# Performance work log

Measured on AMD Instinct MI355X. Metric: run time of the kernel, lower is better.

## Reference

```python
import jax, jax.numpy as jnp
import numpy as np

B, L, D = 8, 4096, 256
G, K = 64, 8          # n_groups, group_size
N = G * K             # 512 slots
H = 8                 # attention heads
EPS = 1e-5

def _ln(x, g, b):
    m = jnp.mean(x, axis=-1, keepdims=True)
    v = jnp.var(x, axis=-1, keepdims=True)
    return (x - m) * jax.lax.rsqrt(v + EPS) * g + b

def _gelu(x):
    return jax.nn.gelu(x, approximate=False)  # torch nn.GELU default = exact erf

def setup_inputs() -> dict:
    key = jax.random.key(0)
    ks = jax.random.split(key, 24)
    s = 0.02
    d = {
        'X': jax.random.normal(ks[0], (B, L, D), jnp.float32),
        'S': jax.random.normal(ks[1], (B, N, D), jnp.float32),
        'Wg':  jax.random.normal(ks[2], (D, G)) * s,
        'Wk':  jax.random.normal(ks[3], (D, K)) * s,
        'Wm1': jax.random.normal(ks[4], (D, 2*D)) * s, 'bm1': jnp.zeros((2*D,)),
        'Wm2': jax.random.normal(ks[5], (2*D, D)) * s, 'bm2': jnp.zeros((D,)),
        'Wgt1': jax.random.normal(ks[6], (D, D)) * s, 'bgt1': jnp.zeros((D,)),
        'Wgt2': jax.random.normal(ks[7], (D, 1)) * s, 'bgt2': jnp.zeros((1,)),
        'Wqkv': jax.random.normal(ks[8], (D, 3*D)) * s, 'bqkv': jnp.zeros((3*D,)),
        'Wo':  jax.random.normal(ks[9], (D, D)) * s, 'bo': jnp.zeros((D,)),
        'aln_g': jnp.ones((D,)), 'aln_b': jnp.zeros((D,)),
        'Wu1': jax.random.normal(ks[10], (2*D, 2*D)) * s, 'bu1': jnp.zeros((2*D,)),
        'Wu2': jax.random.normal(ks[11], (2*D, D)) * s, 'bu2': jnp.zeros((D,)),
        'ln_g': jnp.ones((D,)), 'ln_b': jnp.zeros((D,)),
    }
    return d

def reference(X, S, Wg, Wk, Wm1, bm1, Wm2, bm2, Wgt1, bgt1, Wgt2, bgt2,
              Wqkv, bqkv, Wo, bo, aln_g, aln_b, Wu1, bu1, Wu2, bu2, ln_g, ln_b):
    # --- hierarchical routing (eval path: argmax one-hot) ---
    msg = _gelu(X @ Wm1 + bm1) @ Wm2 + bm2                 # (B,L,D)
    gate = jax.nn.sigmoid(_gelu(X @ Wgt1 + bgt1) @ Wgt2 + bgt2)  # (B,L,1)
    gm = msg * gate
    gidx = jnp.argmax(X @ Wg, axis=-1)                     # (B,L)
    kidx = jnp.argmax(X @ Wk, axis=-1)                     # (B,L)
    idx = gidx * K + kidx                                  # flat slot id in [0,N)
    full = jax.nn.one_hot(idx, N, dtype=X.dtype)           # (B,L,N)
    incoming = jnp.einsum('bln,bld->bnd', full, gm)        # (B,N,D)
    # --- slot self-attention ---
    qkv = S @ Wqkv + bqkv
    q, k, v = jnp.split(qkv, 3, axis=-1)
    dh = D // H
    q = q.reshape(B, N, H, dh); k = k.reshape(B, N, H, dh); v = v.reshape(B, N, H, dh)
    scores = jnp.einsum('bqhd,bkhd->bhqk', q, k) / jnp.sqrt(jnp.asarray(dh, X.dtype))
    attn = jax.nn.softmax(scores, axis=-1)
    o = jnp.einsum('bhqk,bkhd->bqhd', attn, v).reshape(B, N, D) @ Wo + bo
    S1 = _ln(S + o, aln_g, aln_b)
    # --- update ---
    cat = jnp.concatenate([S1, incoming], axis=-1)         # (B,N,2D)
    S2 = S1 + _gelu(cat @ Wu1 + bu1) @ Wu2 + bu2
    return _ln(S2, ln_g, ln_b)
```

## Files before the change

kernel.cpp:

```cpp
#include <hip/hip_runtime.h>

typedef __bf16 bf16_t;
typedef __bf16 bf16x8 __attribute__((ext_vector_type(8)));
typedef __bf16 bf16x4v __attribute__((ext_vector_type(4)));
typedef __bf16 bf16x2v __attribute__((ext_vector_type(2)));
typedef float f32x4 __attribute__((ext_vector_type(4)));
typedef unsigned long long u64;

#define LN_EPS 1e-5f

__device__ __forceinline__ float erf_fast(float a) {
  const float t = fabsf(a);
  const float s = a * a;
  float r;
  if (t > 0.921875f) {
    float u;
    r = fmaf(-1.72853470e-5f, t, 3.83197126e-4f);
    u = fmaf(-3.88396438e-3f, t, 2.42546219e-2f);
    r = fmaf(r, s, u);
    r = fmaf(r, t, 1.06777877e-1f);
    r = fmaf(r, t, -6.37245935e-1f);
    r = fmaf(r, t, -1.28717512e-1f);
    r = fmaf(r, t, t);
    r = 1.0f - __expf(-r);
    r = copysignf(r, a);
  } else {
    r = -5.96761703e-4f;
    r = fmaf(r, s, 4.99119423e-3f);
    r = fmaf(r, s, -2.67681349e-2f);
    r = fmaf(r, s, 1.12819925e-1f);
    r = fmaf(r, s, -3.76125336e-1f);
    r = fmaf(r, s, 1.28379166e-1f);
    r = fmaf(r, a, a);
  }
  return r;
}

__device__ __forceinline__ float gelu_f(float x) {
  const float h = 0.5f * x;
  return fmaf(h, erf_fast(x * 0.70710678118654752f), h);
}

__device__ __forceinline__ void async16(const bf16_t* g, bf16_t* l) {
  __builtin_amdgcn_global_load_lds(
      (const __attribute__((address_space(1))) void*)g,
      (__attribute__((address_space(3))) void*)l, 16, 0, 0);
}

__global__ __launch_bounds__(256)
void prep_kernel(const float* __restrict__ X, const float* __restrict__ S,
                 const float* __restrict__ Wg, const float* __restrict__ Wk,
                 const float* __restrict__ Wm1, const float* __restrict__ Wgt1,
                 const float* __restrict__ Wm2, const float* __restrict__ Wqkv,
                 const float* __restrict__ Wo, const float* __restrict__ Wu1,
                 const float* __restrict__ Wu2,
                 bf16_t* __restrict__ Xb, bf16_t* __restrict__ Sb,
                 bf16_t* __restrict__ W1t, bf16_t* __restrict__ W2t,
                 bf16_t* __restrict__ Wqkvt, bf16_t* __restrict__ Wot,
                 bf16_t* __restrict__ Wu1t, bf16_t* __restrict__ Wu2t,
                 float4* __restrict__ zbase)
{
  const int bid = blockIdx.x;
  const int t = threadIdx.x;
  if (bid < 8192) {
    const int i = bid * 256 + t;
    const float4 v = ((const float4*)X)[i];
    bf16x4v o; o[0]=(bf16_t)v.x; o[1]=(bf16_t)v.y; o[2]=(bf16_t)v.z; o[3]=(bf16_t)v.w;
    ((bf16x4v*)Xb)[i] = o;
  } else if (bid < 9216) {
    const int i = (bid - 8192) * 256 + t;
    const float4 v = ((const float4*)S)[i];
    bf16x4v o; o[0]=(bf16_t)v.x; o[1]=(bf16_t)v.y; o[2]=(bf16_t)v.z; o[3]=(bf16_t)v.w;
    ((bf16x4v*)Sb)[i] = o;
  } else if (bid < 10112) {
    const int n = bid - 9216;
    const int k = t;
    float v;
    if (n < 512)      v = Wm1[k * 512 + n];
    else if (n < 768) v = Wgt1[k * 256 + (n - 512)];
    else if (n < 832) v = Wg[k * 64 + (n - 768)];
    else if (n < 840) v = Wk[k * 8 + (n - 832)];
    else              v = 0.f;
    W1t[n * 256 + k] = (bf16_t)v;
  } else if (bid < 10368) {
    const int n = bid - 10112;
    for (int k = t; k < 512; k += 256) W2t[n * 512 + k] = (bf16_t)Wm2[k * 256 + n];
  } else if (bid < 11136) {
    const int n = bid - 10368;
    Wqkvt[n * 256 + t] = (bf16_t)Wqkv[t * 768 + n];
  } else if (bid < 11392) {
    const int n = bid - 11136;
    Wot[n * 256 + t] = (bf16_t)Wo[t * 256 + n];
  } else if (bid < 11904) {
    const int n = bid - 11392;
    for (int k = t; k < 512; k += 256) Wu1t[n * 512 + k] = (bf16_t)Wu1[k * 512 + n];
  } else if (bid < 12160) {
    const int n = bid - 11904;
    for (int k = t; k < 512; k += 256) Wu2t[n * 512 + k] = (bf16_t)Wu2[k * 256 + n];
  } else {
    zbase[(bid - 12160) * 256 + t] = make_float4(0.f, 0.f, 0.f, 0.f);
  }
}

template<int MT, int EPI>
__global__ __launch_bounds__(256)
void gemm_kernel(const bf16_t* __restrict__ A, int lda,
                 const bf16_t* __restrict__ Bt, int K,
                 const float* __restrict__ bias, const float* __restrict__ bias2,
                 void* __restrict__ outp, int ldc,
                 const float* __restrict__ resid, const float* __restrict__ wgt2,
                 float* __restrict__ gatelin, int* __restrict__ idxb,
                 u64* __restrict__ bitmap)
{
  constexpr int BM = MT * 32;
  constexpr int CA = BM * 4;
  const int m0 = blockIdx.x * BM;
  const int by = blockIdx.y;
  const int n0 = by * 128;
  const int t = threadIdx.x;
  const int w = t >> 6;
  const int lane = t & 63;
  const int wr = w >> 1, wc = w & 1;
  const int quad = lane >> 4, l15 = lane & 15;

  __shared__ bf16_t lA[BM * 32];
  __shared__ bf16_t lB[128 * 32];
  __shared__ float sWg[256];
  __shared__ int sKi[128];

  if constexpr (EPI == 1) {
    if (by >= 4 && by < 6) sWg[t] = wgt2[t];
  }

  f32x4 acc[MT][4];
#pragma unroll
  for (int mt = 0; mt < MT; ++mt)
#pragma unroll
    for (int nt = 0; nt < 4; ++nt)
      acc[mt][nt] = (f32x4){0.f, 0.f, 0.f, 0.f};

  for (int k0 = 0; k0 < K; k0 += 32) {
    if constexpr (CA >= 256) {
#pragma unroll
      for (int i = 0; i < CA / 256; ++i) {
        const int c = i * 256 + t;
        async16(A + (size_t)(m0 + (c >> 2)) * lda + k0 + (c & 3) * 8,
                lA + (size_t)(i * 256 + (t & 192)) * 8);
      }
    } else {
      if (t < CA)
        async16(A + (size_t)(m0 + (t >> 2)) * lda + k0 + (t & 3) * 8,
                lA + (size_t)(t & 192) * 8);
    }
#pragma unroll
    for (int i = 0; i < 2; ++i) {
      const int c = i * 256 + t;
      async16(Bt + (size_t)(n0 + (c >> 2)) * K + k0 + (c & 3) * 8,
              lB + (size_t)(i * 256 + (t & 192)) * 8);
    }
    __syncthreads();
    bf16x8 af[MT], bfr[4];
    const int ko = quad * 8;
#pragma unroll
    for (int mt = 0; mt < MT; ++mt)
      af[mt] = *(const bf16x8*)&lA[(wr * MT * 16 + mt * 16 + l15) * 32 + ko];
#pragma unroll
    for (int nt = 0; nt < 4; ++nt)
      bfr[nt] = *(const bf16x8*)&lB[(wc * 64 + nt * 16 + l15) * 32 + ko];
#pragma unroll
    for (int mt = 0; mt < MT; ++mt)
#pragma unroll
      for (int nt = 0; nt < 4; ++nt)
        acc[mt][nt] = __builtin_amdgcn_mfma_f32_16x16x32_bf16(bfr[nt], af[mt], acc[mt][nt], 0, 0, 0);
    __syncthreads();
  }

  if constexpr (EPI == 1) {
    if (by < 4) {
#pragma unroll
      for (int mt = 0; mt < MT; ++mt) {
        const int row = m0 + wr * MT * 16 + mt * 16 + l15;
#pragma unroll
        for (int nt = 0; nt < 4; ++nt) {
          const int colb = n0 + wc * 64 + nt * 16 + quad * 4;
          const float4 bb = *(const float4*)&bias[colb];
          bf16x4v o;
          o[0] = (bf16_t)gelu_f(acc[mt][nt][0] + bb.x);
          o[1] = (bf16_t)gelu_f(acc[mt][nt][1] + bb.y);
          o[2] = (bf16_t)gelu_f(acc[mt][nt][2] + bb.z);
          o[3] = (bf16_t)gelu_f(acc[mt][nt][3] + bb.w);
          *(bf16x4v*)&((bf16_t*)outp)[(size_t)row * 512 + colb] = o;
        }
      }
    } else if (by < 6) {
#pragma unroll
      for (int mt = 0; mt < MT; ++mt) {
        const int row = m0 + wr * MT * 16 + mt * 16 + l15;
        float part = 0.f;
#pragma unroll
        for (int nt = 0; nt < 4; ++nt) {
          const int colb = n0 + wc * 64 + nt * 16 + quad * 4;
          const int c = colb - 512;
          const float4 bb = *(const float4*)&bias2[c];
          part = fmaf(gelu_f(acc[mt][nt][0] + bb.x), sWg[c + 0], part);
          part = fmaf(gelu_f(acc[mt][nt][1] + bb.y), sWg[c + 1], part);
          part = fmaf(gelu_f(acc[mt][nt][2] + bb.z), sWg[c + 2], part);
          part = fmaf(gelu_f(acc[mt][nt][3] + bb.w), sWg[c + 3], part);
        }
        part += __shfl_xor(part, 16, 64);
        part += __shfl_xor(part, 32, 64);
        if (lane < 16) atomicAdd(&gatelin[row], part);
      }
    } else {
      float bv[MT]; int bi[MT];
#pragma unroll
      for (int mt = 0; mt < MT; ++mt) {
        if (wc == 0) {
          float mv = -1e30f; int mi = 0;
#pragma unroll
          for (int nt = 0; nt < 4; ++nt)
#pragma unroll
            for (int j = 0; j < 4; ++j) {
              const int gc = nt * 16 + quad * 4 + j;
              const float v = acc[mt][nt][j];
              if (v > mv || (v == mv && gc < mi)) { mv = v; mi = gc; }
            }
#pragma unroll
          for (int off = 16; off <= 32; off <<= 1) {
            const float ov = __shfl_xor(mv, off, 64);
            const int oi = __shfl_xor(mi, off, 64);
            if (ov > mv || (ov == mv && oi < mi)) { mv = ov; mi = oi; }
          }
          bv[mt] = mv; bi[mt] = mi;
        } else {
          float mv = -1e30f; int mi = 0;
          if (quad < 2) {
#pragma unroll
            for (int j = 0; j < 4; ++j) {
              const int kc = quad * 4 + j;
              const float v = acc[mt][0][j];
              if (v > mv || (v == mv && kc < mi)) { mv = v; mi = kc; }
            }
          }
#pragma unroll
          for (int off = 16; off <= 32; off <<= 1) {
            const float ov = __shfl_xor(mv, off, 64);
            const int oi = __shfl_xor(mi, off, 64);
            if (ov > mv || (ov == mv && oi < mi)) { mv = ov; mi = oi; }
          }
          if (lane < 16) sKi[wr * MT * 16 + mt * 16 + l15] = mi;
        }
      }
      __syncthreads();
      if (wc == 0 && lane < 16) {
#pragma unroll
        for (int mt = 0; mt < MT; ++mt) {
          const int rl = wr * MT * 16 + mt * 16 + l15;
          const int row = m0 + rl;
          const int idx = bi[mt] * 8 + sKi[rl];
          idxb[row] = idx;
          const int b = row >> 12, tok = row & 4095;
          atomicOr(&bitmap[(size_t)(b * 512 + idx) * 64 + (tok >> 6)],
                   1ull << (tok & 63));
        }
      }
    }
  } else {
#pragma unroll
    for (int mt = 0; mt < MT; ++mt) {
      const int row = m0 + wr * MT * 16 + mt * 16 + l15;
#pragma unroll
      for (int nt = 0; nt < 4; ++nt) {
        const int colb = n0 + wc * 64 + nt * 16 + quad * 4;
        const float4 bb = *(const float4*)&bias[colb];
        float v0 = acc[mt][nt][0] + bb.x, v1 = acc[mt][nt][1] + bb.y;
        float v2 = acc[mt][nt][2] + bb.z, v3 = acc[mt][nt][3] + bb.w;
        if constexpr (EPI == 4) {
          *(float4*)&((float*)outp)[(size_t)row * ldc + colb] = make_float4(v0, v1, v2, v3);
        } else if constexpr (EPI == 5) {
          bf16x4v o; o[0]=(bf16_t)gelu_f(v0); o[1]=(bf16_t)gelu_f(v1);
          o[2]=(bf16_t)gelu_f(v2); o[3]=(bf16_t)gelu_f(v3);
          *(bf16x4v*)&((bf16_t*)outp)[(size_t)row * ldc + colb] = o;
        } else {
          const float4 rr = *(const float4*)&resid[(size_t)row * ldc + colb];
          *(float4*)&((float*)outp)[(size_t)row * ldc + colb] =
              make_float4(v0 + rr.x, v1 + rr.y, v2 + rr.z, v3 + rr.w);
        }
      }
    }
  }
}

__global__ __launch_bounds__(256)
void gemm_pair_kernel(const bf16_t* __restrict__ H, const bf16_t* __restrict__ W2t,
                      const float* __restrict__ bm2, const float* __restrict__ sumg,
                      float* __restrict__ incom,
                      const bf16_t* __restrict__ Sb, const bf16_t* __restrict__ Wqkvt,
                      const float* __restrict__ bqkv, bf16_t* __restrict__ qkvb)
{
  int id = blockIdx.x;
  const bool first = id < 256;
  if (!first) id -= 256;
  const bf16_t* A  = first ? H : Sb;
  const bf16_t* Bt = first ? W2t : Wqkvt;
  const float* bias = first ? bm2 : bqkv;
  const int lda = first ? 512 : 256;
  const int K   = first ? 512 : 256;
  const int ldc = first ? 256 : 768;
  const int m0 = (id & 127) * 32;
  const int n0 = (id >> 7) * 128;
  const int t = threadIdx.x;
  const int w = t >> 6;
  const int lane = t & 63;
  const int wr = w >> 1, wc = w & 1;
  const int quad = lane >> 4, l15 = lane & 15;

  __shared__ bf16_t lA[32 * 32];
  __shared__ bf16_t lB[128 * 32];

  f32x4 acc[4];
#pragma unroll
  for (int nt = 0; nt < 4; ++nt) acc[nt] = (f32x4){0.f, 0.f, 0.f, 0.f};

  for (int k0 = 0; k0 < K; k0 += 32) {
    if (t < 128)
      async16(A + (size_t)(m0 + (t >> 2)) * lda + k0 + (t & 3) * 8,
              lA + (size_t)(t & 192) * 8);
#pragma unroll
    for (int i = 0; i < 2; ++i) {
      const int c = i * 256 + t;
      async16(Bt + (size_t)(n0 + (c >> 2)) * K + k0 + (c & 3) * 8,
              lB + (size_t)(i * 256 + (t & 192)) * 8);
    }
    __syncthreads();
    bf16x8 af, bfr[4];
    const int ko = quad * 8;
    af = *(const bf16x8*)&lA[(wr * 16 + l15) * 32 + ko];
#pragma unroll
    for (int nt = 0; nt < 4; ++nt)
      bfr[nt] = *(const bf16x8*)&lB[(wc * 64 + nt * 16 + l15) * 32 + ko];
#pragma unroll
    for (int nt = 0; nt < 4; ++nt)
      acc[nt] = __builtin_amdgcn_mfma_f32_16x16x32_bf16(bfr[nt], af, acc[nt], 0, 0, 0);
    __syncthreads();
  }

  const int row = m0 + wr * 16 + l15;
  if (first) {
    const float gt = sumg[row];
#pragma unroll
    for (int nt = 0; nt < 4; ++nt) {
      const int colb = n0 + wc * 64 + nt * 16 + quad * 4;
      const float4 bb = *(const float4*)&bias[colb];
      *(float4*)&incom[(size_t)row * ldc + colb] =
          make_float4(fmaf(gt, bb.x, acc[nt][0]), fmaf(gt, bb.y, acc[nt][1]),
                      fmaf(gt, bb.z, acc[nt][2]), fmaf(gt, bb.w, acc[nt][3]));
    }
  } else {
#pragma unroll
    for (int nt = 0; nt < 4; ++nt) {
      const int colb = n0 + wc * 64 + nt * 16 + quad * 4;
      const float4 bb = *(const float4*)&bias[colb];
      bf16x4v o; o[0]=(bf16_t)(acc[nt][0]+bb.x); o[1]=(bf16_t)(acc[nt][1]+bb.y);
      o[2]=(bf16_t)(acc[nt][2]+bb.z); o[3]=(bf16_t)(acc[nt][3]+bb.w);
      *(bf16x4v*)&qkvb[(size_t)row * ldc + colb] = o;
    }
  }
}

__global__ __launch_bounds__(256)
void gather_kernel(const bf16_t* __restrict__ h1, const float* __restrict__ gatelin,
                   const float* __restrict__ bgt2, const u64* __restrict__ bitmap,
                   bf16_t* __restrict__ H, float* __restrict__ sumg)
{
  const int bs = blockIdx.x;
  const int b = bs >> 9;
  const int t = threadIdx.x;
  __shared__ u64 sw[64];
  if (t < 64) sw[t] = bitmap[(size_t)bs * 64 + t];
  __syncthreads();
  const float bg = bgt2[0];
  float a0 = 0.f, a1 = 0.f, sg = 0.f;
  for (int wd = 0; wd < 64; ++wd) {
    u64 word = sw[wd];
    while (word) {
      const int bit = __builtin_ctzll(word);
      word &= word - 1;
      const int l = (b << 12) + (wd << 6) + bit;
      const float g = 1.0f / (1.0f + __expf(-(gatelin[l] + bg)));
      const bf16x2v hv = *(const bf16x2v*)&h1[(size_t)l * 512 + t * 2];
      a0 = fmaf(g, (float)hv[0], a0);
      a1 = fmaf(g, (float)hv[1], a1);
      sg += g;
    }
  }
  bf16x2v o; o[0] = (bf16_t)a0; o[1] = (bf16_t)a1;
  *(bf16x2v*)&H[(size_t)bs * 512 + t * 2] = o;
  if (t == 0) sumg[bs] = sg;
}

__global__ __launch_bounds__(256)
void attn_kernel(const bf16_t* __restrict__ qkv, bf16_t* __restrict__ obuf)
{
  const int bid = blockIdx.x;
  const int qc = bid & 15;
  const int h = (bid >> 4) & 7;
  const int b = bid >> 7;
  const int t = threadIdx.x;
  const int w = t >> 6, lane = t & 63;
  const int quad = lane >> 4, l15 = lane & 15;

  __shared__ bf16_t sP[32 * 520];
  __shared__ bf16_t sVt[32 * 264];
  __shared__ float sL[32];

  bf16x8 qf[2];
#pragma unroll
  for (int mt = 0; mt < 2; ++mt) {
    const int row = b * 512 + qc * 32 + mt * 16 + l15;
    qf[mt] = *(const bf16x8*)&qkv[(size_t)row * 768 + h * 32 + quad * 8];
  }
  const float scale = 0.17677669529663687f;
  for (int kt = w; kt < 32; kt += 4) {
    const int key = b * 512 + kt * 16 + l15;
    const bf16x8 kf = *(const bf16x8*)&qkv[(size_t)key * 768 + 256 + h * 32 + quad * 8];
#pragma unroll
    for (int mt = 0; mt < 2; ++mt) {
      f32x4 c = (f32x4){0.f, 0.f, 0.f, 0.f};
      c = __builtin_amdgcn_mfma_f32_16x16x32_bf16(qf[mt], kf, c, 0, 0, 0);
#pragma unroll
      for (int r = 0; r < 4; ++r)
        sP[(mt * 16 + quad * 4 + r) * 520 + kt * 16 + l15] = (bf16_t)(c[r] * scale);
    }
  }
  __syncthreads();

#pragma unroll
  for (int ri = 0; ri < 8; ++ri) {
    const int row = w * 8 + ri;
    const bf16x8 sv = *(const bf16x8*)&sP[row * 520 + lane * 8];
    float sval[8];
    float mx = -1e30f;
#pragma unroll
    for (int j = 0; j < 8; ++j) { sval[j] = (float)sv[j]; mx = fmaxf(mx, sval[j]); }
#pragma unroll
    for (int off = 32; off; off >>= 1) mx = fmaxf(mx, __shfl_xor(mx, off, 64));
    float sum = 0.f;
    bf16x8 pv;
#pragma unroll
    for (int j = 0; j < 8; ++j) { const float e = __expf(sval[j] - mx); sum += e; pv[j] = (bf16_t)e; }
#pragma unroll
    for (int off = 32; off; off >>= 1) sum += __shfl_xor(sum, off, 64);
    *(bf16x8*)&sP[row * 520 + lane * 8] = pv;
    if (lane == 0) sL[row] = sum;
  }
  __syncthreads();

  const int omt = w >> 1, ont = w & 1;
  f32x4 oacc = (f32x4){0.f, 0.f, 0.f, 0.f};
  for (int half = 0; half < 2; ++half) {
    if (half) __syncthreads();
#pragma unroll
    for (int i = 0; i < 32; ++i) {
      const int el = i * 256 + t;
      const int dh = el & 31, key = el >> 5;
      sVt[dh * 264 + key] = qkv[(size_t)(b * 512 + half * 256 + key) * 768 + 512 + h * 32 + dh];
    }
    __syncthreads();
#pragma unroll
    for (int kt = 0; kt < 8; ++kt) {
      const bf16x8 af = *(const bf16x8*)&sP[(omt * 16 + l15) * 520 + half * 256 + kt * 32 + quad * 8];
      const bf16x8 vf = *(const bf16x8*)&sVt[(ont * 16 + l15) * 264 + kt * 32 + quad * 8];
      oacc = __builtin_amdgcn_mfma_f32_16x16x32_bf16(af, vf, oacc, 0, 0, 0);
    }
  }
#pragma unroll
  for (int r = 0; r < 4; ++r) {
    const int row = omt * 16 + quad * 4 + r;
    const float val = oacc[r] / sL[row];
    obuf[(size_t)(b * 512 + qc * 32 + row) * 256 + h * 32 + ont * 16 + l15] = (bf16_t)val;
  }
}

__global__ __launch_bounds__(256)
void ln1_kernel(const float* __restrict__ S, const float* __restrict__ o2,
                const float* __restrict__ incom, const float* __restrict__ g,
                const float* __restrict__ bb, float* __restrict__ S1f,
                bf16_t* __restrict__ A4)
{
  const int w = threadIdx.x >> 6, lane = threadIdx.x & 63;
  const int row = blockIdx.x * 4 + w;
  const size_t base = (size_t)row * 256 + lane * 4;
  const float4 xs = *(const float4*)&S[base];
  const float4 xo = *(const float4*)&o2[base];
  float x[4] = {xs.x + xo.x, xs.y + xo.y, xs.z + xo.z, xs.w + xo.w};
  float sum = x[0] + x[1] + x[2] + x[3];
  float sq = x[0]*x[0] + x[1]*x[1] + x[2]*x[2] + x[3]*x[3];
#pragma unroll
  for (int off = 32; off; off >>= 1) { sum += __shfl_xor(sum, off, 64); sq += __shfl_xor(sq, off, 64); }
  const float mean = sum * 0.00390625f;
  const float var = sq * 0.00390625f - mean * mean;
  const float rstd = rsqrtf(var + LN_EPS);
  const float4 gg = *(const float4*)&g[lane * 4];
  const float4 bv = *(const float4*)&bb[lane * 4];
  float y[4];
  y[0] = (x[0]-mean)*rstd*gg.x + bv.x;
  y[1] = (x[1]-mean)*rstd*gg.y + bv.y;
  y[2] = (x[2]-mean)*rstd*gg.z + bv.z;
  y[3] = (x[3]-mean)*rstd*gg.w + bv.w;
  *(float4*)&S1f[base] = make_float4(y[0], y[1], y[2], y[3]);
  bf16x4v yb; yb[0]=(bf16_t)y[0]; yb[1]=(bf16_t)y[1]; yb[2]=(bf16_t)y[2]; yb[3]=(bf16_t)y[3];
  *(bf16x4v*)&A4[(size_t)row * 512 + lane * 4] = yb;
  const float4 ic = *(const float4*)&incom[base];
  bf16x4v ib; ib[0]=(bf16_t)ic.x; ib[1]=(bf16_t)ic.y; ib[2]=(bf16_t)ic.z; ib[3]=(bf16_t)ic.w;
  *(bf16x4v*)&A4[(size_t)row * 512 + 256 + lane * 4] = ib;
}

__global__ __launch_bounds__(256)
void ln2_kernel(const float* __restrict__ S2, const float* __restrict__ g,
                const float* __restrict__ bb, float* __restrict__ out)
{
  const int w = threadIdx.x >> 6, lane = threadIdx.x & 63;
  const int row = blockIdx.x * 4 + w;
  const size_t base = (size_t)row * 256 + lane * 4;
  const float4 xv = *(const float4*)&S2[base];
  float x[4] = {xv.x, xv.y, xv.z, xv.w};
  float sum = x[0] + x[1] + x[2] + x[3];
  float sq = x[0]*x[0] + x[1]*x[1] + x[2]*x[2] + x[3]*x[3];
#pragma unroll
  for (int off = 32; off; off >>= 1) { sum += __shfl_xor(sum, off, 64); sq += __shfl_xor(sq, off, 64); }
  const float mean = sum * 0.00390625f;
  const float var = sq * 0.00390625f - mean * mean;
  const float rstd = rsqrtf(var + LN_EPS);
  const float4 gg = *(const float4*)&g[lane * 4];
  const float4 bv = *(const float4*)&bb[lane * 4];
  float4 o;
  o.x = (x[0]-mean)*rstd*gg.x + bv.x;
  o.y = (x[1]-mean)*rstd*gg.y + bv.y;
  o.z = (x[2]-mean)*rstd*gg.z + bv.z;
  o.w = (x[3]-mean)*rstd*gg.w + bv.w;
  *(float4*)&out[base] = o;
}

extern "C" void kernel_launch(void* const* d_in, const int* in_sizes, int n_in,
                              void* d_out, int out_size, void* d_ws, size_t ws_size,
                              hipStream_t stream)
{
  (void)in_sizes; (void)n_in; (void)out_size; (void)ws_size;
  const float* X    = (const float*)d_in[0];
  const float* S    = (const float*)d_in[1];
  const float* Wg   = (const float*)d_in[2];
  const float* Wk   = (const float*)d_in[3];
  const float* Wm1  = (const float*)d_in[4];
  const float* bm1  = (const float*)d_in[5];
  const float* Wm2  = (const float*)d_in[6];
  const float* bm2  = (const float*)d_in[7];
  const float* Wgt1 = (const float*)d_in[8];
  const float* bgt1 = (const float*)d_in[9];
  const float* Wgt2 = (const float*)d_in[10];
  const float* bgt2 = (const float*)d_in[11];
  const float* Wqkv = (const float*)d_in[12];
  const float* bqkv = (const float*)d_in[13];
  const float* Wo   = (const float*)d_in[14];
  const float* bo   = (const float*)d_in[15];
  const float* alng = (const float*)d_in[16];
  const float* alnb = (const float*)d_in[17];
  const float* Wu1  = (const float*)d_in[18];
  const float* bu1  = (const float*)d_in[19];
  const float* Wu2  = (const float*)d_in[20];
  const float* bu2  = (const float*)d_in[21];
  const float* lng  = (const float*)d_in[22];
  const float* lnb  = (const float*)d_in[23];

  char* p = (char*)d_ws;
  auto carve = [&](size_t bytes) { char* r = p; p += bytes; return r; };
  bf16_t* Xb    = (bf16_t*)carve(16777216);
  bf16_t* Sb    = (bf16_t*)carve(2097152);
  bf16_t* W1t   = (bf16_t*)carve(458752);
  bf16_t* W2t   = (bf16_t*)carve(262144);
  bf16_t* Wqkvt = (bf16_t*)carve(393216);
  bf16_t* Wot   = (bf16_t*)carve(131072);
  bf16_t* Wu1t  = (bf16_t*)carve(524288);
  bf16_t* Wu2t  = (bf16_t*)carve(262144);
  bf16_t* h1    = (bf16_t*)carve(33554432);
  u64*    bitmap  = (u64*)carve(2097152);
  float*  gatelin = (float*)carve(131072);
  int*    idxb  = (int*)carve(131072);
  float*  incom = (float*)carve(4194304);
  bf16_t* qkvb  = (bf16_t*)carve(6291456);
  bf16_t* obuf  = (bf16_t*)carve(2097152);
  float*  o2    = (float*)carve(4194304);
  float*  S1f   = (float*)carve(4194304);
  bf16_t* A4    = (bf16_t*)carve(4194304);
  bf16_t* U     = (bf16_t*)carve(4194304);
  float*  S2    = (float*)carve(4194304);
  float*  sumg  = (float*)carve(16384);
  bf16_t* H = U;

  prep_kernel<<<12704, 256, 0, stream>>>(X, S, Wg, Wk, Wm1, Wgt1, Wm2, Wqkv, Wo, Wu1, Wu2,
                                         Xb, Sb, W1t, W2t, Wqkvt, Wot, Wu1t, Wu2t,
                                         (float4*)bitmap);
  gemm_kernel<4,1><<<dim3(256,7), 256, 0, stream>>>(Xb, 256, W1t, 256, bm1, bgt1, h1, 512,
                                                    nullptr, Wgt2, gatelin, idxb, bitmap);
  gather_kernel<<<4096, 256, 0, stream>>>(h1, gatelin, bgt2, bitmap, H, sumg);
  gemm_pair_kernel<<<1024, 256, 0, stream>>>(H, W2t, bm2, sumg, incom,
                                             Sb, Wqkvt, bqkv, qkvb);
  attn_kernel<<<1024, 256, 0, stream>>>(qkvb, obuf);
  gemm_kernel<1,4><<<dim3(128,2), 256, 0, stream>>>(obuf, 256, Wot, 256, bo, nullptr, o2, 256,
                                                    nullptr, nullptr, nullptr, nullptr, nullptr);
  ln1_kernel<<<1024, 256, 0, stream>>>(S, o2, incom, alng, alnb, S1f, A4);
  gemm_kernel<1,5><<<dim3(128,4), 256, 0, stream>>>(A4, 512, Wu1t, 512, bu1, nullptr, U, 512,
                                                    nullptr, nullptr, nullptr, nullptr, nullptr);
  gemm_kernel<1,6><<<dim3(128,2), 256, 0, stream>>>(U, 512, Wu2t, 512, bu2, nullptr, S2, 256,
                                                    S1f, nullptr, nullptr, nullptr, nullptr);
  ln2_kernel<<<1024, 256, 0, stream>>>(S2, lng, lnb, (float*)d_out);
}
```

Before: 271.8 us.

## Fuse Wo and Wu2 GEMMs with their LayerNorms and shrink routing GEMM tile

Replaces the Wo GEMM plus ln1 kernel, and the Wu2 GEMM plus ln2 kernel, with two fused kernels. Each fused kernel computes a 16-row by full-256-column tile so the LayerNorm row reduction runs in the GEMM epilogue, which removes the o2 and S2 intermediate round trips and two launches. The first routing GEMM moves from MT=4 to MT=2 tiles, doubling its grid. The unused idxb output is dropped. The fused kernels launch only 256 blocks with single-buffered loads, which may underuse the GPU.

```diff
diff --git a/kernel.cpp b/kernel.cpp
--- a/kernel.cpp
+++ b/kernel.cpp
@@ -108,8 +108,7 @@
                  const bf16_t* __restrict__ Bt, int K,
                  const float* __restrict__ bias, const float* __restrict__ bias2,
                  void* __restrict__ outp, int ldc,
-                 const float* __restrict__ resid, const float* __restrict__ wgt2,
-                 float* __restrict__ gatelin, int* __restrict__ idxb,
+                 const float* __restrict__ wgt2, float* __restrict__ gatelin,
                  u64* __restrict__ bitmap)
 {
   constexpr int BM = MT * 32;
@@ -126,7 +125,7 @@
   __shared__ bf16_t lA[BM * 32];
   __shared__ bf16_t lB[128 * 32];
   __shared__ float sWg[256];
-  __shared__ int sKi[128];
+  __shared__ int sKi[BM];
 
   if constexpr (EPI == 1) {
     if (by >= 4 && by < 6) sWg[t] = wgt2[t];
@@ -212,7 +211,7 @@
         if (lane < 16) atomicAdd(&gatelin[row], part);
       }
     } else {
-      float bv[MT]; int bi[MT];
+      int bi[MT];
 #pragma unroll
       for (int mt = 0; mt < MT; ++mt) {
         if (wc == 0) {
@@ -231,7 +230,7 @@
             const int oi = __shfl_xor(mi, off, 64);
             if (ov > mv || (ov == mv && oi < mi)) { mv = ov; mi = oi; }
           }
-          bv[mt] = mv; bi[mt] = mi;
+          bi[mt] = mi;
         } else {
           float mv = -1e30f; int mi = 0;
           if (quad < 2) {
@@ -258,7 +257,6 @@
           const int rl = wr * MT * 16 + mt * 16 + l15;
           const int row = m0 + rl;
           const int idx = bi[mt] * 8 + sKi[rl];
-          idxb[row] = idx;
           const int b = row >> 12, tok = row & 4095;
           atomicOr(&bitmap[(size_t)(b * 512 + idx) * 64 + (tok >> 6)],
                    1ull << (tok & 63));
@@ -273,19 +271,10 @@
       for (int nt = 0; nt < 4; ++nt) {
         const int colb = n0 + wc * 64 + nt * 16 + quad * 4;
         const float4 bb = *(const float4*)&bias[colb];
-        float v0 = acc[mt][nt][0] + bb.x, v1 = acc[mt][nt][1] + bb.y;
-        float v2 = acc[mt][nt][2] + bb.z, v3 = acc[mt][nt][3] + bb.w;
-        if constexpr (EPI == 4) {
-          *(float4*)&((float*)outp)[(size_t)row * ldc + colb] = make_float4(v0, v1, v2, v3);
-        } else if constexpr (EPI == 5) {
-          bf16x4v o; o[0]=(bf16_t)gelu_f(v0); o[1]=(bf16_t)gelu_f(v1);
-          o[2]=(bf16_t)gelu_f(v2); o[3]=(bf16_t)gelu_f(v3);
-          *(bf16x4v*)&((bf16_t*)outp)[(size_t)row * ldc + colb] = o;
-        } else {
-          const float4 rr = *(const float4*)&resid[(size_t)row * ldc + colb];
-          *(float4*)&((float*)outp)[(size_t)row * ldc + colb] =
-              make_float4(v0 + rr.x, v1 + rr.y, v2 + rr.z, v3 + rr.w);
-        }
+        bf16x4v o;
+        o[0]=(bf16_t)gelu_f(acc[mt][nt][0]+bb.x); o[1]=(bf16_t)gelu_f(acc[mt][nt][1]+bb.y);
+        o[2]=(bf16_t)gelu_f(acc[mt][nt][2]+bb.z); o[3]=(bf16_t)gelu_f(acc[mt][nt][3]+bb.w);
+        *(bf16x4v*)&((bf16_t*)outp)[(size_t)row * ldc + colb] = o;
       }
     }
   }
@@ -483,63 +472,157 @@
 }
 
 __global__ __launch_bounds__(256)
-void ln1_kernel(const float* __restrict__ S, const float* __restrict__ o2,
-                const float* __restrict__ incom, const float* __restrict__ g,
-                const float* __restrict__ bb, float* __restrict__ S1f,
-                bf16_t* __restrict__ A4)
-{
-  const int w = threadIdx.x >> 6, lane = threadIdx.x & 63;
-  const int row = blockIdx.x * 4 + w;
-  const size_t base = (size_t)row * 256 + lane * 4;
-  const float4 xs = *(const float4*)&S[base];
-  const float4 xo = *(const float4*)&o2[base];
-  float x[4] = {xs.x + xo.x, xs.y + xo.y, xs.z + xo.z, xs.w + xo.w};
-  float sum = x[0] + x[1] + x[2] + x[3];
-  float sq = x[0]*x[0] + x[1]*x[1] + x[2]*x[2] + x[3]*x[3];
-#pragma unroll
-  for (int off = 32; off; off >>= 1) { sum += __shfl_xor(sum, off, 64); sq += __shfl_xor(sq, off, 64); }
-  const float mean = sum * 0.00390625f;
-  const float var = sq * 0.00390625f - mean * mean;
+void wo_ln1_kernel(const bf16_t* __restrict__ obuf, const bf16_t* __restrict__ Wot,
+                   const float* __restrict__ bo, const float* __restrict__ S,
+                   const float* __restrict__ incom, const float* __restrict__ g,
+                   const float* __restrict__ bb, float* __restrict__ S1f,
+                   bf16_t* __restrict__ A4)
+{
+  const int m0 = blockIdx.x * 16;
+  const int t = threadIdx.x;
+  const int w = t >> 6, lane = t & 63;
+  const int quad = lane >> 4, l15 = lane & 15;
+
+  __shared__ bf16_t lA[16 * 32];
+  __shared__ bf16_t lB[256 * 32];
+  __shared__ float sSum[4][16];
+  __shared__ float sSq[4][16];
+
+  f32x4 acc[4];
+#pragma unroll
+  for (int nt = 0; nt < 4; ++nt) acc[nt] = (f32x4){0.f, 0.f, 0.f, 0.f};
+
+  for (int k0 = 0; k0 < 256; k0 += 32) {
+    if (t < 64)
+      async16(obuf + (size_t)(m0 + (t >> 2)) * 256 + k0 + (t & 3) * 8, lA);
+#pragma unroll
+    for (int i = 0; i < 4; ++i) {
+      const int c = i * 256 + t;
+      async16(Wot + (size_t)(c >> 2) * 256 + k0 + (c & 3) * 8,
+              lB + (size_t)(i * 256 + (t & 192)) * 8);
+    }
+    __syncthreads();
+    const int ko = quad * 8;
+    const bf16x8 af = *(const bf16x8*)&lA[l15 * 32 + ko];
+#pragma unroll
+    for (int nt = 0; nt < 4; ++nt) {
+      const bf16x8 bfr = *(const bf16x8*)&lB[(w * 64 + nt * 16 + l15) * 32 + ko];
+      acc[nt] = __builtin_amdgcn_mfma_f32_16x16x32_bf16(bfr, af, acc[nt], 0, 0, 0);
+    }
+    __syncthreads();
+  }
+
+  const int row = m0 + l15;
+  float sum = 0.f, sq = 0.f;
+#pragma unroll
+  for (int nt = 0; nt < 4; ++nt) {
+    const int colb = w * 64 + nt * 16 + quad * 4;
+    const float4 bv = *(const float4*)&bo[colb];
+    const float4 sv = *(const float4*)&S[(size_t)row * 256 + colb];
+    float x0 = acc[nt][0] + bv.x + sv.x, x1 = acc[nt][1] + bv.y + sv.y;
+    float x2 = acc[nt][2] + bv.z + sv.z, x3 = acc[nt][3] + bv.w + sv.w;
+    acc[nt][0] = x0; acc[nt][1] = x1; acc[nt][2] = x2; acc[nt][3] = x3;
+    sum += x0 + x1 + x2 + x3;
+    sq += x0*x0 + x1*x1 + x2*x2 + x3*x3;
+  }
+  sum += __shfl_xor(sum, 16, 64); sum += __shfl_xor(sum, 32, 64);
+  sq  += __shfl_xor(sq, 16, 64);  sq  += __shfl_xor(sq, 32, 64);
+  if (lane < 16) { sSum[w][l15] = sum; sSq[w][l15] = sq; }
+  __syncthreads();
+  const float tot = sSum[0][l15] + sSum[1][l15] + sSum[2][l15] + sSum[3][l15];
+  const float tq  = sSq[0][l15] + sSq[1][l15] + sSq[2][l15] + sSq[3][l15];
+  const float mean = tot * 0.00390625f;
+  const float var = tq * 0.00390625f - mean * mean;
   const float rstd = rsqrtf(var + LN_EPS);
-  const float4 gg = *(const float4*)&g[lane * 4];
-  const float4 bv = *(const float4*)&bb[lane * 4];
-  float y[4];
-  y[0] = (x[0]-mean)*rstd*gg.x + bv.x;
-  y[1] = (x[1]-mean)*rstd*gg.y + bv.y;
-  y[2] = (x[2]-mean)*rstd*gg.z + bv.z;
-  y[3] = (x[3]-mean)*rstd*gg.w + bv.w;
-  *(float4*)&S1f[base] = make_float4(y[0], y[1], y[2], y[3]);
-  bf16x4v yb; yb[0]=(bf16_t)y[0]; yb[1]=(bf16_t)y[1]; yb[2]=(bf16_t)y[2]; yb[3]=(bf16_t)y[3];
-  *(bf16x4v*)&A4[(size_t)row * 512 + lane * 4] = yb;
-  const float4 ic = *(const float4*)&incom[base];
-  bf16x4v ib; ib[0]=(bf16_t)ic.x; ib[1]=(bf16_t)ic.y; ib[2]=(bf16_t)ic.z; ib[3]=(bf16_t)ic.w;
-  *(bf16x4v*)&A4[(size_t)row * 512 + 256 + lane * 4] = ib;
+#pragma unroll
+  for (int nt = 0; nt < 4; ++nt) {
+    const int colb = w * 64 + nt * 16 + quad * 4;
+    const float4 gg = *(const float4*)&g[colb];
+    const float4 bv = *(const float4*)&bb[colb];
+    const float y0 = (acc[nt][0]-mean)*rstd*gg.x + bv.x;
+    const float y1 = (acc[nt][1]-mean)*rstd*gg.y + bv.y;
+    const float y2 = (acc[nt][2]-mean)*rstd*gg.z + bv.z;
+    const float y3 = (acc[nt][3]-mean)*rstd*gg.w + bv.w;
+    *(float4*)&S1f[(size_t)row * 256 + colb] = make_float4(y0, y1, y2, y3);
+    bf16x4v yb; yb[0]=(bf16_t)y0; yb[1]=(bf16_t)y1; yb[2]=(bf16_t)y2; yb[3]=(bf16_t)y3;
+    *(bf16x4v*)&A4[(size_t)row * 512 + colb] = yb;
+    const float4 ic = *(const float4*)&incom[(size_t)row * 256 + colb];
+    bf16x4v ib; ib[0]=(bf16_t)ic.x; ib[1]=(bf16_t)ic.y; ib[2]=(bf16_t)ic.z; ib[3]=(bf16_t)ic.w;
+    *(bf16x4v*)&A4[(size_t)row * 512 + 256 + colb] = ib;
+  }
 }
 
 __global__ __launch_bounds__(256)
-void ln2_kernel(const float* __restrict__ S2, const float* __restrict__ g,
-                const float* __restrict__ bb, float* __restrict__ out)
-{
-  const int w = threadIdx.x >> 6, lane = threadIdx.x & 63;
-  const int row = blockIdx.x * 4 + w;
-  const size_t base = (size_t)row * 256 + lane * 4;
-  const float4 xv = *(const float4*)&S2[base];
-  float x[4] = {xv.x, xv.y, xv.z, xv.w};
-  float sum = x[0] + x[1] + x[2] + x[3];
-  float sq = x[0]*x[0] + x[1]*x[1] + x[2]*x[2] + x[3]*x[3];
-#pragma unroll
-  for (int off = 32; off; off >>= 1) { sum += __shfl_xor(sum, off, 64); sq += __shfl_xor(sq, off, 64); }
-  const float mean = sum * 0.00390625f;
-  const float var = sq * 0.00390625f - mean * mean;
+void wu2_ln2_kernel(const bf16_t* __restrict__ U, const bf16_t* __restrict__ Wu2t,
+                    const float* __restrict__ bu2, const float* __restrict__ S1f,
+                    const float* __restrict__ g, const float* __restrict__ bb,
+                    float* __restrict__ out)
+{
+  const int m0 = blockIdx.x * 16;
+  const int t = threadIdx.x;
+  const int w = t >> 6, lane = t & 63;
+  const int quad = lane >> 4, l15 = lane & 15;
+
+  __shared__ bf16_t lA[16 * 32];
+  __shared__ bf16_t lB[256 * 32];
+  __shared__ float sSum[4][16];
+  __shared__ float sSq[4][16];
+
+  f32x4 acc[4];
+#pragma unroll
+  for (int nt = 0; nt < 4; ++nt) acc[nt] = (f32x4){0.f, 0.f, 0.f, 0.f};
+
+  for (int k0 = 0; k0 < 512; k0 += 32) {
+    if (t < 64)
+      async16(U + (size_t)(m0 + (t >> 2)) * 512 + k0 + (t & 3) * 8, lA);
+#pragma unroll
+    for (int i = 0; i < 4; ++i) {
+      const int c = i * 256 + t;
+      async16(Wu2t + (size_t)(c >> 2) * 512 + k0 + (c & 3) * 8,
+              lB + (size_t)(i * 256 + (t & 192)) * 8);
+    }
+    __syncthreads();
+    const int ko = quad * 8;
+    const bf16x8 af = *(const bf16x8*)&lA[l15 * 32 + ko];
+#pragma unroll
+    for (int nt = 0; nt < 4; ++nt) {
+      const bf16x8 bfr = *(const bf16x8*)&lB[(w * 64 + nt * 16 + l15) * 32 + ko];
+      acc[nt] = __builtin_amdgcn_mfma_f32_16x16x32_bf16(bfr, af, acc[nt], 0, 0, 0);
+    }
+    __syncthreads();
+  }
+
+  const int row = m0 + l15;
+  float sum = 0.f, sq = 0.f;
+#pragma unroll
+  for (int nt = 0; nt < 4; ++nt) {
+    const int colb = w * 64 + nt * 16 + quad * 4;
+    const float4 bv = *(const float4*)&bu2[colb];
+    const float4 sv = *(const float4*)&S1f[(size_t)row * 256 + colb];
+    float x0 = acc[nt][0] + bv.x + sv.x, x1 = acc[nt][1] + bv.y + sv.y;
+    float x2 = acc[nt][2] + bv.z + sv.z, x3 = acc[nt][3] + bv.w + sv.w;
+    acc[nt][0] = x0; acc[nt][1] = x1; acc[nt][2] = x2; acc[nt][3] = x3;
+    sum += x0 + x1 + x2 + x3;
+    sq += x0*x0 + x1*x1 + x2*x2 + x3*x3;
+  }
+  sum += __shfl_xor(sum, 16, 64); sum += __shfl_xor(sum, 32, 64);
+  sq  += __shfl_xor(sq, 16, 64);  sq  += __shfl_xor(sq, 32, 64);
+  if (lane < 16) { sSum[w][l15] = sum; sSq[w][l15] = sq; }
+  __syncthreads();
+  const float tot = sSum[0][l15] + sSum[1][l15] + sSum[2][l15] + sSum[3][l15];
+  const float tq  = sSq[0][l15] + sSq[1][l15] + sSq[2][l15] + sSq[3][l15];
+  const float mean = tot * 0.00390625f;
+  const float var = tq * 0.00390625f - mean * mean;
   const float rstd = rsqrtf(var + LN_EPS);
-  const float4 gg = *(const float4*)&g[lane * 4];
-  const float4 bv = *(const float4*)&bb[lane * 4];
-  float4 o;
-  o.x = (x[0]-mean)*rstd*gg.x + bv.x;
-  o.y = (x[1]-mean)*rstd*gg.y + bv.y;
-  o.z = (x[2]-mean)*rstd*gg.z + bv.z;
-  o.w = (x[3]-mean)*rstd*gg.w + bv.w;
-  *(float4*)&out[base] = o;
+#pragma unroll
+  for (int nt = 0; nt < 4; ++nt) {
+    const int colb = w * 64 + nt * 16 + quad * 4;
+    const float4 gg = *(const float4*)&g[colb];
+    const float4 bv = *(const float4*)&bb[colb];
+    *(float4*)&out[(size_t)row * 256 + colb] = make_float4(
+        (acc[nt][0]-mean)*rstd*gg.x + bv.x, (acc[nt][1]-mean)*rstd*gg.y + bv.y,
+        (acc[nt][2]-mean)*rstd*gg.z + bv.z, (acc[nt][3]-mean)*rstd*gg.w + bv.w);
+  }
 }
 
 extern "C" void kernel_launch(void* const* d_in, const int* in_sizes, int n_in,
@@ -585,33 +668,26 @@
   bf16_t* h1    = (bf16_t*)carve(33554432);
   u64*    bitmap  = (u64*)carve(2097152);
   float*  gatelin = (float*)carve(131072);
-  int*    idxb  = (int*)carve(131072);
   float*  incom = (float*)carve(4194304);
   bf16_t* qkvb  = (bf16_t*)carve(6291456);
   bf16_t* obuf  = (bf16_t*)carve(2097152);
-  float*  o2    = (float*)carve(4194304);
   float*  S1f   = (float*)carve(4194304);
   bf16_t* A4    = (bf16_t*)carve(4194304);
   bf16_t* U     = (bf16_t*)carve(4194304);
-  float*  S2    = (float*)carve(4194304);
   float*  sumg  = (float*)carve(16384);
   bf16_t* H = U;
 
   prep_kernel<<<12704, 256, 0, stream>>>(X, S, Wg, Wk, Wm1, Wgt1, Wm2, Wqkv, Wo, Wu1, Wu2,
                                          Xb, Sb, W1t, W2t, Wqkvt, Wot, Wu1t, Wu2t,
                                          (float4*)bitmap);
-  gemm_kernel<4,1><<<dim3(256,7), 256, 0, stream>>>(Xb, 256, W1t, 256, bm1, bgt1, h1, 512,
-                                                    nullptr, Wgt2, gatelin, idxb, bitmap);
+  gemm_kernel<2,1><<<dim3(512,7), 256, 0, stream>>>(Xb, 256, W1t, 256, bm1, bgt1, h1, 512,
+                                                    Wgt2, gatelin, bitmap);
   gather_kernel<<<4096, 256, 0, stream>>>(h1, gatelin, bgt2, bitmap, H, sumg);
   gemm_pair_kernel<<<1024, 256, 0, stream>>>(H, W2t, bm2, sumg, incom,
                                              Sb, Wqkvt, bqkv, qkvb);
   attn_kernel<<<1024, 256, 0, stream>>>(qkvb, obuf);
-  gemm_kernel<1,4><<<dim3(128,2), 256, 0, stream>>>(obuf, 256, Wot, 256, bo, nullptr, o2, 256,
-                                                    nullptr, nullptr, nullptr, nullptr, nullptr);
-  ln1_kernel<<<1024, 256, 0, stream>>>(S, o2, incom, alng, alnb, S1f, A4);
+  wo_ln1_kernel<<<256, 256, 0, stream>>>(obuf, Wot, bo, S, incom, alng, alnb, S1f, A4);
   gemm_kernel<1,5><<<dim3(128,4), 256, 0, stream>>>(A4, 512, Wu1t, 512, bu1, nullptr, U, 512,
-                                                    nullptr, nullptr, nullptr, nullptr, nullptr);
-  gemm_kernel<1,6><<<dim3(128,2), 256, 0, stream>>>(U, 512, Wu2t, 512, bu2, nullptr, S2, 256,
-                                                    S1f, nullptr, nullptr, nullptr, nullptr);
-  ln2_kernel<<<1024, 256, 0, stream>>>(S2, lng, lnb, (float*)d_out);
-}
+                                                    nullptr, nullptr, nullptr);
+  wu2_ln2_kernel<<<256, 256, 0, stream>>>(U, Wu2t, bu2, S1f, lng, lnb, (float*)d_out);
+}
```

After: 260.9 us. 4.0% less time.
